# Kernel optimization log

Hardware: AMD Instinct MI355X
Metric: run time of the kernel (lower is better)

## Reference

```python
import jax, jax.numpy as jnp
import numpy as np

LMAX = 10
F_IN = 64
F_OUT = 64
N_GRID = 512
B = 512


def setup_inputs() -> dict:
    key = jax.random.key(0)
    k1, k2, k3 = jax.random.split(key, 3)
    x = jax.random.normal(k1, (B, F_IN, (LMAX + 1) ** 2), dtype=jnp.float32)
    w = jax.random.normal(k2, (F_IN, F_OUT, N_GRID), dtype=jnp.float32)
    Y = jax.random.normal(k3, (N_GRID, (LMAX + 1) ** 2), dtype=jnp.float32)
    return {"x": x, "w": w, "Y": Y}


def reference(x, w, Y):
    # Project spatial filter into harmonic (fourier) domain.
    # psi: (f_in, f_out, (lmax+1)^2), one scalar weight per (l, u) output mult slot
    n_grid = Y.shape[0]
    psi = jnp.einsum('ni,xyn->xyi', Y, w) / (n_grid ** 0.5)

    lmax = int(round(Y.shape[1] ** 0.5)) - 1
    f_in = w.shape[0]
    f_out = w.shape[1]
    alpha = 1.0 / (f_in ** 0.5)  # e3nn Linear path normalization (mul_in=1)

    outs = []
    for l in range(lmax + 1):  # structural loop over irrep degrees (11 blocks)
        d = 2 * l + 1
        xs = x[:, :, l * l:(l + 1) * (l + 1)]     # (B, f_in, d)  single input copy of irrep l
        ws = psi[:, :, l * l:(l + 1) * (l + 1)]    # (f_in, f_out, d) -> d = output multiplicity u
        # out block: (B, f_out, mult=d, m=d)
        o = jnp.einsum('egu,bem->bgum', ws, xs) * alpha
        outs.append(o.reshape(x.shape[0], f_out, d * d))
    return jnp.concatenate(outs, axis=-1)  # (B, f_out, sum_l (2l+1)^2)
```

## Files before the change

kernel.cpp:

```cpp
#include <hip/hip_runtime.h>
#include <hip/hip_bf16.h>


#define OUTROW 1771
#define OUTB   113344

typedef __attribute__((ext_vector_type(8))) short bf16x8;
typedef __attribute__((ext_vector_type(4))) float floatx4;

__device__ __constant__ int c_blk[12] = {0,2,30,96,216,406,705,1137,1633,2403,3283,4229};
__device__ __constant__ signed char c_ltab[121] = {
  0,
  1,1,1,
  2,2,2,2,2,
  3,3,3,3,3,3,3,
  4,4,4,4,4,4,4,4,4,
  5,5,5,5,5,5,5,5,5,5,5,
  6,6,6,6,6,6,6,6,6,6,6,6,6,
  7,7,7,7,7,7,7,7,7,7,7,7,7,7,7,
  8,8,8,8,8,8,8,8,8,8,8,8,8,8,8,8,8,
  9,9,9,9,9,9,9,9,9,9,9,9,9,9,9,9,9,9,9,
  10,10,10,10,10,10,10,10,10,10,10,10,10,10,10,10,10,10,10,10,10
};

__global__ __launch_bounds__(256) void prep_kernel(
    const float* __restrict__ x, const float* __restrict__ w,
    const float* __restrict__ Y,
    __hip_bfloat16* __restrict__ psi_t, __hip_bfloat16* __restrict__ x_t)
{
  __shared__ float smem[8256];
  const int t = threadIdx.x;

  if (blockIdx.x < 64) {
    const int g    = blockIdx.x;
    const int wv   = t >> 6, lane = t & 63;
    const int ln15 = lane & 15, quad = lane >> 4;

    floatx4 acc[2][4] = {};

    for (int n0 = 0; n0 < 512; n0 += 64) {
      __syncthreads();
      {
        const float4* src = (const float4*)(Y + n0*121);
        float4* dst = (float4*)smem;
        for (int idx = t; idx < 1936; idx += 256) dst[idx] = src[idx];
      }
      __syncthreads();

      #pragma unroll
      for (int ks = 0; ks < 2; ++ks) {
        const int kb = ks*32 + quad*8;

        bf16x8 ahi[2], alo[2];
        #pragma unroll
        for (int ti = 0; ti < 2; ++ti) {
          const int irow = (wv << 5) + (ti << 4) + ln15;
          #pragma unroll
          for (int j = 0; j < 8; ++j) {
            float v = smem[(kb + j)*121 + irow];
            __hip_bfloat16 h = __float2bfloat16(v);
            float hf = __bfloat162float(h);
            __hip_bfloat16 lo = __float2bfloat16(v - hf);
            ahi[ti][j] = *(short*)&h;
            alo[ti][j] = *(short*)&lo;
          }
        }

        bf16x8 bhi[4], blo[4];
        #pragma unroll
        for (int te = 0; te < 4; ++te) {
          const int e = (te << 4) + ln15;
          const float* wp = w + ((e << 6) + g)*512 + n0 + kb;
          float4 wa = *(const float4*)wp;
          float4 wb = *(const float4*)(wp + 4);
          float v[8] = {wa.x, wa.y, wa.z, wa.w, wb.x, wb.y, wb.z, wb.w};
          #pragma unroll
          for (int j = 0; j < 8; ++j) {
            __hip_bfloat16 h = __float2bfloat16(v[j]);
            float hf = __bfloat162float(h);
            __hip_bfloat16 lo = __float2bfloat16(v[j] - hf);
            bhi[te][j] = *(short*)&h;
            blo[te][j] = *(short*)&lo;
          }
        }

        #pragma unroll
        for (int ti = 0; ti < 2; ++ti) {
          #pragma unroll
          for (int te = 0; te < 4; ++te) {
            acc[ti][te] = __builtin_amdgcn_mfma_f32_16x16x32_bf16(ahi[ti], bhi[te], acc[ti][te], 0, 0, 0);
            acc[ti][te] = __builtin_amdgcn_mfma_f32_16x16x32_bf16(ahi[ti], blo[te], acc[ti][te], 0, 0, 0);
            acc[ti][te] = __builtin_amdgcn_mfma_f32_16x16x32_bf16(alo[ti], bhi[te], acc[ti][te], 0, 0, 0);
          }
        }
      }
    }

    const float scale = 0.00552427172801990267f;
    #pragma unroll
    for (int ti = 0; ti < 2; ++ti) {
      #pragma unroll
      for (int rr = 0; rr < 4; ++rr) {
        const int i = (wv << 5) + (ti << 4) + (quad << 2) + rr;
        if (i < 121) {
          int l = c_ltab[i];
          int d = 2*l + 1;
          int row = 64*l*l + g*d + (i - l*l);
          #pragma unroll
          for (int te = 0; te < 4; ++te) {
            __hip_bfloat16 hv = __float2bfloat16(acc[ti][te][rr] * scale);
            psi_t[row*64 + (te << 4) + ln15] = hv;
          }
        }
      }
    }
  } else {
    const int b = blockIdx.x - 64;
    {
      const float4* src = (const float4*)(x + b*7744);
      float4* dst = (float4*)smem;
      for (int idx = t; idx < 1936; idx += 256) dst[idx] = src[idx];
    }
    __syncthreads();
    const int wv = t >> 6, lane = t & 63;
    for (int ii = wv; ii < 121; ii += 4) {
      int l = c_ltab[ii];
      int d = 2*l + 1;
      int row = 512*l*l + b*d + (ii - l*l);
      x_t[row*64 + lane] = __float2bfloat16(smem[lane*121 + ii]);
    }
  }
}

#define LPITCH 258

template <int L>
__device__ void conv_body(int r, int t,
                          const ushort* __restrict__ psi,
                          const ushort* __restrict__ xt,
                          float* __restrict__ out, float* lt)
{
  constexpr int d    = 2*L + 1;
  constexpr int dd   = d*d;
  constexpr int GT   = 64  / d;
  constexpr int BT   = 256 / d;
  constexpr int NBT  = (512 + BT - 1) / BT;
  constexpr int OFFL = L*(2*L - 1)*(2*L + 1)/3;

  const int wv = t >> 6, lane = t & 63;
  const int wslot = wv & 3, qhalf = wv >> 2;
  const int ln15 = lane & 15, quad = lane >> 4;

  const int gtI = r / NBT;
  const int btI = r - gtI*NBT;
  const int g0 = gtI*GT, b0 = btI*BT;

  int pr = g0*d + wslot*16 + ln15;
  if (pr > 64*d - 1) pr = 64*d - 1;
  const ushort* psiRow = psi + (64*L*L + pr)*64 + quad*8;
  const bf16x8 af0 = *(const bf16x8*)(psiRow);
  const bf16x8 af1 = *(const bf16x8*)(psiRow + 32);

  const ushort* xbase = xt + 512*L*L*64 + quad*8;

  #pragma unroll 4
  for (int qi = 0; qi < 8; ++qi) {
    const int qq = qhalf*8 + qi;
    int qr = b0*d + qq*16 + ln15;
    if (qr > 512*d - 1) qr = 512*d - 1;
    const ushort* xr = xbase + qr*64;
    bf16x8 bf0 = *(const bf16x8*)(xr);
    bf16x8 bf1 = *(const bf16x8*)(xr + 32);
    floatx4 acc = {0.f, 0.f, 0.f, 0.f};
    acc = __builtin_amdgcn_mfma_f32_16x16x32_bf16(af0, bf0, acc, 0, 0, 0);
    acc = __builtin_amdgcn_mfma_f32_16x16x32_bf16(af1, bf1, acc, 0, 0, 0);
    float* dst = lt + (wslot*16 + quad*4)*LPITCH + qq*16 + ln15;
    #pragma unroll
    for (int rr = 0; rr < 4; ++rr) dst[rr*LPITCH] = acc[rr];
  }
  __syncthreads();

  if constexpr (dd >= 64) {
    for (int pp = wv; pp < GT*BT; pp += 8) {
      const int g_i = pp / BT;
      const int b_i = pp - g_i*BT;
      const int g = g0 + g_i, b = b0 + b_i;
      if (g >= 64 || b >= 512) continue;
      const int obase = b*OUTB + g*OUTROW + OFFL;
      const float* lrow = lt + (g_i*d)*LPITCH + b_i*d;
      #pragma unroll
      for (int o0 = 0; o0 < dd; o0 += 64) {
        int o = o0 + lane;
        if (o < dd) {
          int u = o / d;
          int m = o - u*d;
          out[obase + o] = lrow[u*LPITCH + m];
        }
      }
    }
  } else {
    constexpr int PPI = 64 / dd;
    const int pq = lane / dd;
    const int o  = lane - pq*dd;
    const int u  = o / d;
    const int m  = o - u*d;
    for (int base = wv*PPI; base < GT*BT; base += 8*PPI) {
      int pp = base + pq;
      if (pq < PPI && pp < GT*BT) {
        int g_i = pp / BT;
        int b_i = pp - g_i*BT;
        int g = g0 + g_i, b = b0 + b_i;
        if (g < 64 && b < 512)
          out[b*OUTB + g*OUTROW + OFFL + o] = lt[(g_i*d + u)*LPITCH + b_i*d + m];
      }
    }
  }
}

__global__ __launch_bounds__(512) void conv_kernel(
    const __hip_bfloat16* __restrict__ psi_t,
    const __hip_bfloat16* __restrict__ x_t,
    float* __restrict__ out)
{
  __shared__ float lt[64*LPITCH];

  const int orig = blockIdx.x;
  const int xcd = orig & 7, idx = orig >> 3;
  const int bid = (xcd < 5 ? xcd*529 : 2645 + (xcd - 5)*528) + idx;

  int l = 0;
  #pragma unroll
  for (int ll = 1; ll <= 10; ++ll)
    if (bid >= c_blk[ll]) l = ll;
  const int r = bid - c_blk[l];

  const ushort* psi = (const ushort*)psi_t;
  const ushort* xt  = (const ushort*)x_t;
  const int t = threadIdx.x;

  switch (l) {
    case 0:  conv_body<0 >(r, t, psi, xt, out, lt); break;
    case 1:  conv_body<1 >(r, t, psi, xt, out, lt); break;
    case 2:  conv_body<2 >(r, t, psi, xt, out, lt); break;
    case 3:  conv_body<3 >(r, t, psi, xt, out, lt); break;
    case 4:  conv_body<4 >(r, t, psi, xt, out, lt); break;
    case 5:  conv_body<5 >(r, t, psi, xt, out, lt); break;
    case 6:  conv_body<6 >(r, t, psi, xt, out, lt); break;
    case 7:  conv_body<7 >(r, t, psi, xt, out, lt); break;
    case 8:  conv_body<8 >(r, t, psi, xt, out, lt); break;
    case 9:  conv_body<9 >(r, t, psi, xt, out, lt); break;
    default: conv_body<10>(r, t, psi, xt, out, lt); break;
  }
}

extern "C" void kernel_launch(void* const* d_in, const int* in_sizes, int n_in,
                              void* d_out, int out_size, void* d_ws, size_t ws_size,
                              hipStream_t stream) {
  const float* x = (const float*)d_in[0];
  const float* w = (const float*)d_in[1];
  const float* Y = (const float*)d_in[2];
  float* out = (float*)d_out;

  __hip_bfloat16* psi_t = (__hip_bfloat16*)d_ws;
  __hip_bfloat16* x_t   = (__hip_bfloat16*)((char*)d_ws + (1 << 20));

  prep_kernel<<<576, 256, 0, stream>>>(x, w, Y, psi_t, x_t);
  conv_kernel<<<4229, 512, 0, stream>>>(psi_t, x_t, out);
}
```

Measured before the change: 358.3 us.

## Stage operands in swizzled LDS and store MFMA results directly to output

The conv kernel now loads psi and x tiles cooperatively into XOR-swizzled shared memory, and waves read their MFMA fragments from there instead of doing scattered per-lane global loads. The output is written straight from the accumulators with precomputed row offsets and bounds masks, dropping the float LDS transpose buffer and its second pass. This cuts LDS traffic and one barrier. In exchange the global stores are less coalesced, since each lane scatters four floats across output rows instead of writing contiguous d*d blocks.

```diff
diff --git a/kernel.cpp b/kernel.cpp
--- a/kernel.cpp
+++ b/kernel.cpp
@@ -132,20 +132,19 @@
   }
 }
 
-#define LPITCH 258
-
 template <int L>
 __device__ void conv_body(int r, int t,
                           const ushort* __restrict__ psi,
                           const ushort* __restrict__ xt,
-                          float* __restrict__ out, float* lt)
+                          float* __restrict__ out, ushort* sm)
 {
   constexpr int d    = 2*L + 1;
-  constexpr int dd   = d*d;
   constexpr int GT   = 64  / d;
   constexpr int BT   = 256 / d;
   constexpr int NBT  = (512 + BT - 1) / BT;
   constexpr int OFFL = L*(2*L - 1)*(2*L + 1)/3;
+  constexpr int PMAXR = 64*d  - 1;
+  constexpr int QMAXR = 512*d - 1;
 
   const int wv = t >> 6, lane = t & 63;
   const int wslot = wv & 3, qhalf = wv >> 2;
@@ -154,66 +153,63 @@
   const int gtI = r / NBT;
   const int btI = r - gtI*NBT;
   const int g0 = gtI*GT, b0 = btI*BT;
-
-  int pr = g0*d + wslot*16 + ln15;
-  if (pr > 64*d - 1) pr = 64*d - 1;
-  const ushort* psiRow = psi + (64*L*L + pr)*64 + quad*8;
-  const bf16x8 af0 = *(const bf16x8*)(psiRow);
-  const bf16x8 af1 = *(const bf16x8*)(psiRow + 32);
-
-  const ushort* xbase = xt + 512*L*L*64 + quad*8;
-
-  #pragma unroll 4
+  const int p0 = g0*d, q0 = b0*d;
+
+  const ushort* psiSec = psi + 64*L*L*64;
+  const ushort* xSec   = xt + 512*L*L*64;
+
+  ushort* smA = sm;
+  ushort* smB = sm + 4096;
+
+  {
+    const int row = t >> 3, slot = t & 7;
+    int prow = p0 + row; if (prow > PMAXR) prow = PMAXR;
+    bf16x8 v = *(const bf16x8*)(psiSec + prow*64 + slot*8);
+    *(bf16x8*)(smA + row*64 + (((slot ^ (row & 7))) << 3)) = v;
+  }
+  #pragma unroll
+  for (int cc = 0; cc < 4; ++cc) {
+    const int c = cc*512 + t;
+    const int row = c >> 3, slot = c & 7;
+    int qrow = q0 + row; if (qrow > QMAXR) qrow = QMAXR;
+    bf16x8 v = *(const bf16x8*)(xSec + qrow*64 + slot*8);
+    *(bf16x8*)(smB + row*64 + (((slot ^ (row & 7))) << 3)) = v;
+  }
+  __syncthreads();
+
+  const int ar = wslot*16 + ln15;
+  const bf16x8 af0 = *(const bf16x8*)(smA + ar*64 + (((quad    ) ^ (ar & 7)) << 3));
+  const bf16x8 af1 = *(const bf16x8*)(smA + ar*64 + (((quad + 4) ^ (ar & 7)) << 3));
+
+  const int plim = (g0 + GT < 64 ? g0 + GT : 64) * d;
+  const int qlim = (b0 + BT < 512 ? b0 + BT : 512) * d;
+  int rowoff[4]; bool pok[4];
+  #pragma unroll
+  for (int rr = 0; rr < 4; ++rr) {
+    const int p_abs = p0 + wslot*16 + quad*4 + rr;
+    const int gg = p_abs / d;
+    const int uu = p_abs - gg*d;
+    rowoff[rr] = gg*OUTROW + uu*d;
+    pok[rr] = p_abs < plim;
+  }
+
+  #pragma unroll
   for (int qi = 0; qi < 8; ++qi) {
     const int qq = qhalf*8 + qi;
-    int qr = b0*d + qq*16 + ln15;
-    if (qr > 512*d - 1) qr = 512*d - 1;
-    const ushort* xr = xbase + qr*64;
-    bf16x8 bf0 = *(const bf16x8*)(xr);
-    bf16x8 bf1 = *(const bf16x8*)(xr + 32);
+    const int br = qq*16 + ln15;
+    bf16x8 bf0 = *(const bf16x8*)(smB + br*64 + (((quad    ) ^ (br & 7)) << 3));
+    bf16x8 bf1 = *(const bf16x8*)(smB + br*64 + (((quad + 4) ^ (br & 7)) << 3));
     floatx4 acc = {0.f, 0.f, 0.f, 0.f};
     acc = __builtin_amdgcn_mfma_f32_16x16x32_bf16(af0, bf0, acc, 0, 0, 0);
     acc = __builtin_amdgcn_mfma_f32_16x16x32_bf16(af1, bf1, acc, 0, 0, 0);
-    float* dst = lt + (wslot*16 + quad*4)*LPITCH + qq*16 + ln15;
+    const int q_abs = q0 + br;
+    const int bb = q_abs / d;
+    const int mm = q_abs - bb*d;
+    const bool qok = q_abs < qlim;
+    const int obase = bb*OUTB + OFFL + mm;
     #pragma unroll
-    for (int rr = 0; rr < 4; ++rr) dst[rr*LPITCH] = acc[rr];
-  }
-  __syncthreads();
-
-  if constexpr (dd >= 64) {
-    for (int pp = wv; pp < GT*BT; pp += 8) {
-      const int g_i = pp / BT;
-      const int b_i = pp - g_i*BT;
-      const int g = g0 + g_i, b = b0 + b_i;
-      if (g >= 64 || b >= 512) continue;
-      const int obase = b*OUTB + g*OUTROW + OFFL;
-      const float* lrow = lt + (g_i*d)*LPITCH + b_i*d;
-      #pragma unroll
-      for (int o0 = 0; o0 < dd; o0 += 64) {
-        int o = o0 + lane;
-        if (o < dd) {
-          int u = o / d;
-          int m = o - u*d;
-          out[obase + o] = lrow[u*LPITCH + m];
-        }
-      }
-    }
-  } else {
-    constexpr int PPI = 64 / dd;
-    const int pq = lane / dd;
-    const int o  = lane - pq*dd;
-    const int u  = o / d;
-    const int m  = o - u*d;
-    for (int base = wv*PPI; base < GT*BT; base += 8*PPI) {
-      int pp = base + pq;
-      if (pq < PPI && pp < GT*BT) {
-        int g_i = pp / BT;
-        int b_i = pp - g_i*BT;
-        int g = g0 + g_i, b = b0 + b_i;
-        if (g < 64 && b < 512)
-          out[b*OUTB + g*OUTROW + OFFL + o] = lt[(g_i*d + u)*LPITCH + b_i*d + m];
-      }
-    }
+    for (int rr = 0; rr < 4; ++rr)
+      if (qok && pok[rr]) out[obase + rowoff[rr]] = acc[rr];
   }
 }
 
@@ -222,7 +218,7 @@
     const __hip_bfloat16* __restrict__ x_t,
     float* __restrict__ out)
 {
-  __shared__ float lt[64*LPITCH];
+  __shared__ __align__(16) ushort sm[20480];
 
   const int orig = blockIdx.x;
   const int xcd = orig & 7, idx = orig >> 3;
@@ -239,17 +235,17 @@
   const int t = threadIdx.x;
 
   switch (l) {
-    case 0:  conv_body<0 >(r, t, psi, xt, out, lt); break;
-    case 1:  conv_body<1 >(r, t, psi, xt, out, lt); break;
-    case 2:  conv_body<2 >(r, t, psi, xt, out, lt); break;
-    case 3:  conv_body<3 >(r, t, psi, xt, out, lt); break;
-    case 4:  conv_body<4 >(r, t, psi, xt, out, lt); break;
-    case 5:  conv_body<5 >(r, t, psi, xt, out, lt); break;
-    case 6:  conv_body<6 >(r, t, psi, xt, out, lt); break;
-    case 7:  conv_body<7 >(r, t, psi, xt, out, lt); break;
-    case 8:  conv_body<8 >(r, t, psi, xt, out, lt); break;
-    case 9:  conv_body<9 >(r, t, psi, xt, out, lt); break;
-    default: conv_body<10>(r, t, psi, xt, out, lt); break;
+    case 0:  conv_body<0 >(r, t, psi, xt, out, sm); break;
+    case 1:  conv_body<1 >(r, t, psi, xt, out, sm); break;
+    case 2:  conv_body<2 >(r, t, psi, xt, out, sm); break;
+    case 3:  conv_body<3 >(r, t, psi, xt, out, sm); break;
+    case 4:  conv_body<4 >(r, t, psi, xt, out, sm); break;
+    case 5:  conv_body<5 >(r, t, psi, xt, out, sm); break;
+    case 6:  conv_body<6 >(r, t, psi, xt, out, sm); break;
+    case 7:  conv_body<7 >(r, t, psi, xt, out, sm); break;
+    case 8:  conv_body<8 >(r, t, psi, xt, out, sm); break;
+    case 9:  conv_body<9 >(r, t, psi, xt, out, sm); break;
+    default: conv_body<10>(r, t, psi, xt, out, sm); break;
   }
 }
 
```

Measured after the change: 337.8 us. -5.7%, faster.
